# Kernel optimization log

Hardware: AMD Instinct MI355X
Metric: run time of the kernel (lower is better)

The kernel has to match this reference:

```python
import jax, jax.numpy as jnp
import numpy as np

U, B, S, R = 64, 256, 256, 512
N = 4096
EMA_DECAY = 0.99


def setup_inputs() -> dict:
    key = jax.random.key(0)
    ks = jax.random.split(key, 9)
    q_u = jax.random.uniform(ks[0], (N, U), dtype=jnp.float32)
    q_b = jax.random.uniform(ks[1], (N, B), dtype=jnp.float32)
    q_sigma = jax.random.normal(ks[2], (N, S), dtype=jnp.float32)
    delta_rule_target = jax.random.normal(ks[3], (N, R), dtype=jnp.float32)
    write_mask = jax.random.randint(ks[4], (N,), 0, 2).astype(bool)
    delta_rule_proto = 0.02 * jax.random.normal(ks[5], (U, B, R), dtype=jnp.float32)
    signature_proto = 0.02 * jax.random.normal(ks[6], (U, B, S), dtype=jnp.float32)
    ema_conf = jax.random.uniform(ks[7], (U, B), dtype=jnp.float32)
    usage_count = jnp.maximum(jax.random.uniform(ks[8], (U, B)) - 0.5, 0.0) * 100.0
    return {"q_u": q_u, "q_b": q_b, "q_sigma": q_sigma,
            "delta_rule_target": delta_rule_target, "write_mask": write_mask,
            "delta_rule_proto": delta_rule_proto, "signature_proto": signature_proto,
            "ema_conf": ema_conf, "usage_count": usage_count}


def _l2norm(x):
    return x / jnp.maximum(jnp.linalg.norm(x, axis=-1, keepdims=True), 1e-12)


def reference(q_u, q_b, q_sigma, delta_rule_target, write_mask,
              delta_rule_proto, signature_proto, ema_conf, usage_count):
    # ---------------- retrieve ----------------
    # joint attention over (operator, binding) cells; temperature == 1.0 branch
    joint = q_u[:, :, None] * q_b[:, None, :]                  # [N, U, B]
    valid = (usage_count > 0).astype(joint.dtype)              # [U, B]
    w = joint * valid
    denom = w.sum(axis=(-2, -1), keepdims=True)
    w = jnp.where(denom > 0, w / jnp.maximum(denom, 1e-6), jnp.zeros_like(w))
    memory_delta_rule = jnp.einsum('nub,ubr->nr', w, delta_rule_proto)
    memory_signature = jnp.einsum('nub,ubs->ns', w, signature_proto)
    base_conf = jnp.einsum('nub,ub->n', w, ema_conf)[:, None]  # [N, 1]
    cos = jnp.sum(_l2norm(q_sigma) * _l2norm(memory_signature + 1e-6),
                  axis=-1, keepdims=True)
    signature_agreement = 0.5 * (1.0 + cos)
    memory_conf = jnp.clip(base_conf * signature_agreement, 0.0, 1.0)

    # ---------------- update (vectorized scatter EMA) ----------------
    m = write_mask.astype(q_u.dtype)                           # [N]
    op_conf = q_u.max(axis=-1)
    op_id = jnp.argmax(q_u, axis=-1)
    bind_conf = q_b.max(axis=-1)
    bind_id = jnp.argmax(q_b, axis=-1)
    write_conf = op_conf * bind_conf                           # [N]
    cell = op_id * B + bind_id                                 # [N]
    num_cells = U * B
    wgt = write_conf * m
    sum_w = jax.ops.segment_sum(wgt, cell, num_segments=num_cells)          # [UB]
    sum_d = jax.ops.segment_sum(delta_rule_target * wgt[:, None], cell,
                                num_segments=num_cells)                     # [UB, R]
    sum_s = jax.ops.segment_sum(q_sigma * wgt[:, None], cell,
                                num_segments=num_cells)                     # [UB, S]
    cnt = jax.ops.segment_sum(m, cell, num_segments=num_cells)              # [UB]
    conf_sum = jnp.maximum(sum_w, 1e-6)
    delta_mean = (sum_d / conf_sum[:, None]).reshape(U, B, R)
    sigma_mean = (sum_s / conf_sum[:, None]).reshape(U, B, S)
    conf_mean = (sum_w / jnp.maximum(cnt, 1.0)).reshape(U, B)
    upd = (cnt > 0).reshape(U, B)
    new_delta_proto = jnp.where(upd[:, :, None],
                                EMA_DECAY * delta_rule_proto + (1.0 - EMA_DECAY) * delta_mean,
                                delta_rule_proto)
    new_signature_proto = jnp.where(upd[:, :, None],
                                    EMA_DECAY * signature_proto + (1.0 - EMA_DECAY) * sigma_mean,
                                    signature_proto)
    new_ema_conf = jnp.where(upd,
                             EMA_DECAY * ema_conf + (1.0 - EMA_DECAY) * conf_mean,
                             ema_conf)
    new_usage = usage_count + cnt.reshape(U, B)

    # ---------------- usage stats ----------------
    write_rate = m.mean()
    usage_fraction = (new_usage > 0).astype(jnp.float32).mean()
    dist = new_usage.reshape(-1)
    dist = dist / jnp.maximum(dist.sum(), 1e-6)
    usage_entropy = -(dist * jnp.log(dist + 1e-6)).sum() / np.log(max(2, num_cells))

    return (memory_delta_rule, memory_signature, memory_conf,
            new_delta_proto, new_signature_proto, new_ema_conf, new_usage,
            write_rate, usage_fraction, usage_entropy)
```

## Files before the change

### kernel.cpp

```cpp
#include <hip/hip_runtime.h>
#include <hip/hip_fp8.h>
#include <math.h>

#define NR 4096
#define UD 64
#define BD 256
#define SD 256
#define RD 512
#define UBD 16384
#define DECAY 0.99f

typedef unsigned char u8;
typedef __attribute__((ext_vector_type(4))) float f32x4;
typedef __attribute__((ext_vector_type(2))) long longx2;

#define OFF_MDR   0ull
#define OFF_MSIG  2097152ull
#define OFF_MCONF 3145728ull
#define OFF_NDP   3149824ull
#define OFF_NSP   11538432ull
#define OFF_NEC   15732736ull
#define OFF_NUS   15749120ull
#define OFF_SCAL  15765504ull

static __device__ __forceinline__ u8 f2e4m3(float x) {
  __hip_fp8_e4m3 h(x);
  return (u8)h.__x;
}

static __device__ __forceinline__ void gll16(const void* g, void* l) {
  __builtin_amdgcn_global_load_lds(
      (const __attribute__((address_space(1))) unsigned int*)g,
      (__attribute__((address_space(3))) unsigned int*)l, 16, 0, 0);
}

static __device__ __forceinline__ int perm64(int x) {
  return (((x >> 3) & 3) << 4) | (((x >> 5) & 1) << 3) | (x & 7);
}

__global__ __launch_bounds__(256) void row_prep_kernel(
    const float* __restrict__ q_u, const float* __restrict__ q_b,
    const float* __restrict__ usage, const float* __restrict__ ema,
    const unsigned char* __restrict__ wm,
    float* __restrict__ denom, float* __restrict__ base_raw,
    float* __restrict__ wgt, int* __restrict__ cellid, float* __restrict__ mrow)
{
  const int r0 = blockIdx.x * 4;
  const int t = threadIdx.x;
  __shared__ float s_qu[4][64];
  __shared__ float s_qbv[4][256];
  __shared__ float s_pd[4][256];
  __shared__ float s_pc[4][256];
  __shared__ int s_flag;
  {
    const int r = t >> 6, u = t & 63;
    s_qu[r][u] = q_u[(size_t)(r0 + r) * UD + u];
  }
  if (t == 0) {
    const int*   wi = (const int*)wm;
    const float* wf = (const float*)wm;
    bool is_i32 = true, is_f32 = true;
    #pragma unroll
    for (int i = 0; i < 16; ++i) {
      int v = wi[i];
      if (v != 0 && v != 1) is_i32 = false;
      float f = wf[i];
      if (f != 0.f && f != 1.f) is_f32 = false;
    }
    s_flag = is_i32 ? 2 : (is_f32 ? 1 : 0);
  }
  #pragma unroll
  for (int r = 0; r < 4; ++r)
    s_qbv[r][t] = q_b[(size_t)(r0 + r) * BD + t];
  __syncthreads();
  float accd[4] = {0.f, 0.f, 0.f, 0.f};
  float accc[4] = {0.f, 0.f, 0.f, 0.f};
  #pragma unroll 4
  for (int u = 0; u < UD; ++u) {
    const float us = usage[u * BD + t];
    const float em = ema[u * BD + t];
    const float vm = (us > 0.f) ? 1.f : 0.f;
    const float ev = em * vm;
    #pragma unroll
    for (int r = 0; r < 4; ++r) {
      accd[r] += s_qu[r][u] * vm;
      accc[r] += s_qu[r][u] * ev;
    }
  }
  #pragma unroll
  for (int r = 0; r < 4; ++r) {
    s_pd[r][t] = accd[r] * s_qbv[r][t];
    s_pc[r][t] = accc[r] * s_qbv[r][t];
  }
  __syncthreads();
  const int w = t >> 6, l = t & 63;
  float dsum = s_pd[w][l] + s_pd[w][l + 64] + s_pd[w][l + 128] + s_pd[w][l + 192];
  float csum = s_pc[w][l] + s_pc[w][l + 64] + s_pc[w][l + 128] + s_pc[w][l + 192];
  #pragma unroll
  for (int m = 1; m < 64; m <<= 1) {
    dsum += __shfl_xor(dsum, m);
    csum += __shfl_xor(csum, m);
  }
  float bv_ = s_qbv[w][l]; int bi_ = l;
  #pragma unroll
  for (int k = 1; k < 4; ++k) {
    const float v2 = s_qbv[w][l + k * 64];
    if (v2 > bv_) { bv_ = v2; bi_ = l + k * 64; }
  }
  #pragma unroll
  for (int m = 1; m < 64; m <<= 1) {
    const float ov = __shfl_xor(bv_, m);
    const int   oi = __shfl_xor(bi_, m);
    if (ov > bv_ || (ov == bv_ && oi < bi_)) { bv_ = ov; bi_ = oi; }
  }
  float uv_ = s_qu[w][l & 63]; int ui_ = l;
  #pragma unroll
  for (int m = 1; m < 64; m <<= 1) {
    const float ov = __shfl_xor(uv_, m);
    const int   oi = __shfl_xor(ui_, m);
    if (ov > uv_ || (ov == uv_ && oi < ui_)) { uv_ = ov; ui_ = oi; }
  }
  if (l == 0) {
    const int n = r0 + w;
    const int fm = s_flag;
    float m;
    if (fm == 2)      m = (((const int*)wm)[n]   != 0)   ? 1.f : 0.f;
    else if (fm == 1) m = (((const float*)wm)[n] != 0.f) ? 1.f : 0.f;
    else              m = (wm[n] != 0)   ? 1.f : 0.f;
    denom[n]    = dsum;
    base_raw[n] = csum;
    wgt[n]      = uv_ * bv_ * m;
    cellid[n]   = ui_ * BD + bi_;
    mrow[n]     = m;
  }
}

__global__ __launch_bounds__(256) void prep_kernel(
    const float* __restrict__ qb, const float* __restrict__ qu,
    u8* __restrict__ qb8, float* __restrict__ quT)
{
  if (blockIdx.x < 1024) {
    const int i = blockIdx.x * 256 + threadIdx.x;
    const int idx = i * 4;
    const int row = idx >> 8;
    const int b   = idx & 255;
    const float4 v = *(const float4*)(qb + (size_t)idx);
    u8 tmp[4] = { f2e4m3(v.x), f2e4m3(v.y), f2e4m3(v.z), f2e4m3(v.w) };
    unsigned int wv; __builtin_memcpy(&wv, tmp, 4);
    const int nb = (b & ~63) | perm64(b & 63);
    *(unsigned int*)(qb8 + (size_t)row * BD + nb) = wv;
  } else {
    __shared__ float s[64][65];
    const int n0 = (blockIdx.x - 1024) * 64;
    const int tid = threadIdx.x;
    #pragma unroll
    for (int i = 0; i < 16; ++i) {
      const int idx = tid + i * 256;
      const int r = idx >> 6, u = idx & 63;
      s[r][u] = qu[(size_t)(n0 + r) * UD + u];
    }
    __syncthreads();
    #pragma unroll
    for (int i = 0; i < 16; ++i) {
      const int idx = tid + i * 256;
      const int u = idx >> 6, r = idx & 63;
      quT[(size_t)u * NR + n0 + r] = s[r][u];
    }
  }
}

__global__ __launch_bounds__(256) void transpose_mask_kernel(
    const float* __restrict__ dproto, const float* __restrict__ sproto,
    const float* __restrict__ usage, u8* __restrict__ PT8)
{
  __shared__ u8 s[64][68];
  const int k0 = blockIdx.x * 64;
  const int rblk = blockIdx.y;
  const float* src; int ld; int c0s;
  if (rblk < 8) { src = dproto; ld = RD; c0s = rblk * 64; }
  else          { src = sproto; ld = SD; c0s = (rblk - 8) * 64; }
  const int tid = threadIdx.x;
  const int kl = tid >> 4;
  const int rl = (tid & 15) * 4;
  #pragma unroll
  for (int i = 0; i < 4; ++i) {
    const int k = kl + i * 16;
    const bool valid = usage[k0 + k] > 0.f;
    const float4 v = *(const float4*)(src + (size_t)(k0 + k) * ld + c0s + rl);
    s[k][rl + 0] = valid ? f2e4m3(v.x) : (u8)0;
    s[k][rl + 1] = valid ? f2e4m3(v.y) : (u8)0;
    s[k][rl + 2] = valid ? f2e4m3(v.z) : (u8)0;
    s[k][rl + 3] = valid ? f2e4m3(v.w) : (u8)0;
  }
  __syncthreads();
  const int rl2 = tid >> 4;
  const int kl2 = (tid & 15) * 4;
  #pragma unroll
  for (int i = 0; i < 4; ++i) {
    const int r = rl2 + i * 16;
    u8 tmp[4] = { s[kl2 + 0][r], s[kl2 + 1][r], s[kl2 + 2][r], s[kl2 + 3][r] };
    unsigned int wv; __builtin_memcpy(&wv, tmp, 4);
    *(unsigned int*)(PT8 + (size_t)(rblk * 64 + r) * UBD + k0 + perm64(kl2)) = wv;
  }
}

__global__ __launch_bounds__(256, 3) void mfma_gemm_kernel(
    const float* __restrict__ quT, const u8* __restrict__ qb8,
    const u8* __restrict__ PT8, float* __restrict__ out,
    int* __restrict__ tk, int* __restrict__ gf, int* __restrict__ claimed)
{
  __shared__ u8 sA[2][128 * 128];
  __shared__ u8 sB[2][128 * 64];
  __shared__ int s_work;
  const int tid = threadIdx.x;

  if (tid == 0) {
    unsigned int xcc;
    asm volatile("s_getreg_b32 %0, hwreg(HW_REG_XCC_ID)" : "=s"(xcc));
    const int x = (int)(xcc & 7u);
    const int t = atomicAdd(&tk[x], 1);
    int w = -1;
    if (t < 96) {
      const int cand = x * 96 + t;
      if (atomicCAS(&claimed[cand], 0, 1) == 0) w = cand;
    }
    while (w < 0) {
      const int g = atomicAdd(gf, 1);
      if (g >= 768) { w = -2; break; }
      if (atomicCAS(&claimed[g], 0, 1) == 0) w = g;
    }
    s_work = w;
  }
  __syncthreads();
  const int w = s_work;
  if (w < 0) return;

  const int bx = w & 31;
  const int combo = w >> 5;
  const int by = combo >> 2;
  const int bz = combo & 3;

  const int wid = tid >> 6, lane = tid & 63;
  const int n0 = bx * 128;
  const int kbeg = bz * (UBD / 4);

  float* obase; int ldO; int cc0;
  if (by < 4) { obase = out + OFF_MDR;  ldO = RD; cc0 = by * 128; }
  else        { obase = out + OFF_MSIG; ldO = SD; cc0 = (by - 4) * 128; }
  const int c0 = by * 128;

  const int lrowA = lane >> 3;
  const int csrcA = ((lane & 7) ^ lrowA) * 16;
  const u8* gA = qb8 + (size_t)(n0 + lrowA) * BD + csrcA;
  const int lrowB = lane >> 2;
  const int srcslotB = (lane & 3) ^ ((lrowB >> 1) & 3);
  const u8* gB = PT8 + (size_t)(c0 + wid * 16 + lrowB) * UBD + kbeg + srcslotB * 16;

  const int wr = (wid >> 1) * 64, wc = (wid & 1) * 64;
  const int fr = lane & 15;
  const int kg = lane >> 4;
  int aoff[4], boff[4];
  #pragma unroll
  for (int m = 0; m < 4; ++m) aoff[m] = (wr + m * 16 + fr) * 128;
  #pragma unroll
  for (int nn = 0; nn < 4; ++nn) boff[nn] = (wc + nn * 16 + fr) * 64;
  int slothA[2];
  #pragma unroll
  for (int bq = 0; bq < 2; ++bq) slothA[bq] = ((bq * 4 + kg) ^ (fr & 7)) * 16;
  const int slotB16 = (kg ^ ((fr >> 1) & 3)) * 16;

  f32x4 accm[4][4];
  #pragma unroll
  for (int m = 0; m < 4; ++m)
    #pragma unroll
    for (int nn = 0; nn < 4; ++nn)
      accm[m][nn] = (f32x4){0.f, 0.f, 0.f, 0.f};

  #pragma unroll
  for (int i = 0; i < 4; ++i) {
    const int ro = wid * 32 + i * 8;
    gll16(gA + (size_t)ro * BD,       &sA[0][ro * 128]);
    gll16(gA + (size_t)ro * BD + 128, &sA[1][ro * 128]);
  }
  #pragma unroll
  for (int i = 0; i < 2; ++i)
    gll16(gB + (size_t)(i * 64) * UBD, &sB[0][(i * 64 + wid * 16) * 64]);
  __syncthreads();

  const float* quTb = quT + n0 + wr + kg * 4;
  const int ubase = kbeg >> 8;
  f32x4 accu[4][4];

  for (int ph = 0; ph < 64; ++ph) {
    const int buf  = ph & 1;
    const int half = (ph >> 1) & 1;
    const int bq   = ph & 1;
    if (ph < 63) {
      const u8* gs = gB + (size_t)(ph + 1) * 64;
      #pragma unroll
      for (int i = 0; i < 2; ++i)
        gll16(gs + (size_t)(i * 64) * UBD, &sB[buf ^ 1][(i * 64 + wid * 16) * 64]);
    }
    const u8* sa = sA[half];
    const u8* sb = sB[buf];
    longx2 av[4], bv[4];
    #pragma unroll
    for (int m = 0; m < 4; ++m)
      av[m] = *(const longx2*)(sa + aoff[m] + slothA[bq]);
    #pragma unroll
    for (int nn = 0; nn < 4; ++nn)
      bv[nn] = *(const longx2*)(sb + boff[nn] + slotB16);
    const bool first = (ph & 3) == 0;
    #pragma unroll
    for (int m = 0; m < 4; ++m)
      #pragma unroll
      for (int nn = 0; nn < 4; ++nn) {
        if (first)
          accu[m][nn] = __builtin_amdgcn_mfma_f32_16x16x32_fp8_fp8(
              av[m].x, bv[nn].x, (f32x4){0.f, 0.f, 0.f, 0.f}, 0, 0, 0);
        else
          accu[m][nn] = __builtin_amdgcn_mfma_f32_16x16x32_fp8_fp8(
              av[m].x, bv[nn].x, accu[m][nn], 0, 0, 0);
        accu[m][nn] = __builtin_amdgcn_mfma_f32_16x16x32_fp8_fp8(
            av[m].y, bv[nn].y, accu[m][nn], 0, 0, 0);
      }
    __syncthreads();
    if ((ph & 3) == 3) {
      const float* qp = quTb + (size_t)(ubase + (ph >> 2)) * NR;
      #pragma unroll
      for (int m = 0; m < 4; ++m) {
        const f32x4 qv = *(const f32x4*)(qp + m * 16);
        #pragma unroll
        for (int nn = 0; nn < 4; ++nn)
          accm[m][nn] += qv * accu[m][nn];
      }
    }
  }

  #pragma unroll
  for (int m = 0; m < 4; ++m) {
    #pragma unroll
    for (int nn = 0; nn < 4; ++nn) {
      const int c = cc0 + wc + nn * 16 + fr;
      #pragma unroll
      for (int j = 0; j < 4; ++j) {
        const int r = n0 + wr + m * 16 + kg * 4 + j;
        atomicAdd(obase + (size_t)r * ldO + c, accm[m][nn][j]);
      }
    }
  }
}

__global__ __launch_bounds__(256) void epilogue_kernel(
    const float* __restrict__ q_sigma, const float* __restrict__ denom,
    const float* __restrict__ base_raw, float* __restrict__ out)
{
  const int n = blockIdx.x;
  const int t = threadIdx.x;
  __shared__ float r1[256], r2[256], r3[256];
  const float d = denom[n];
  const float scale = (d > 0.f) ? (1.f / fmaxf(d, 1e-6f)) : 0.f;
  float* mdr = out + OFF_MDR + (size_t)n * RD;
  mdr[t]       *= scale;
  mdr[t + 256] *= scale;
  float* msig = out + OFF_MSIG + (size_t)n * SD;
  const float s = msig[t] * scale;
  msig[t] = s;
  const float a = q_sigma[(size_t)n * SD + t];
  const float b = s + 1e-6f;
  r1[t] = a * a; r2[t] = b * b; r3[t] = a * b;
  __syncthreads();
  for (int st = 128; st > 0; st >>= 1) {
    if (t < st) { r1[t] += r1[t + st]; r2[t] += r2[t + st]; r3[t] += r3[t + st]; }
    __syncthreads();
  }
  if (t == 0) {
    const float na = fmaxf(sqrtf(r1[0]), 1e-12f);
    const float nb = fmaxf(sqrtf(r2[0]), 1e-12f);
    const float cosv = r3[0] / (na * nb);
    const float agree = 0.5f * (1.f + cosv);
    const float base = (d > 0.f) ? base_raw[n] / fmaxf(d, 1e-6f) : 0.f;
    out[OFF_MCONF + n] = fminf(fmaxf(base * agree, 0.f), 1.f);
  }
}

__global__ __launch_bounds__(256) void small_sums_kernel(
    const float* __restrict__ wgt, const int* __restrict__ cellid,
    const float* __restrict__ mrow,
    float* __restrict__ sum_w, float* __restrict__ cnt)
{
  const int n = blockIdx.x * 256 + threadIdx.x;
  if (n < NR && mrow[n] != 0.f) {
    atomicAdd(&sum_w[cellid[n]], wgt[n]);
    atomicAdd(&cnt[cellid[n]], 1.f);
  }
}

__global__ __launch_bounds__(256) void ema_copy_kernel(
    const float* __restrict__ dproto, const float* __restrict__ sproto,
    const float* __restrict__ cnt,
    float* __restrict__ outd, float* __restrict__ outs)
{
  const size_t nd = (size_t)UBD * RD;
  const size_t total = nd + (size_t)UBD * SD;
  for (size_t i = (size_t)blockIdx.x * 256 + threadIdx.x; i < total;
       i += (size_t)gridDim.x * 256) {
    if (i < nd) {
      const float p = dproto[i];
      outd[i] = (cnt[(int)(i >> 9)] > 0.f) ? DECAY * p : p;
    } else {
      const size_t j = i - nd;
      const float p = sproto[j];
      outs[j] = (cnt[(int)(j >> 8)] > 0.f) ? DECAY * p : p;
    }
  }
}

__global__ __launch_bounds__(256) void scatter2_kernel(
    const float* __restrict__ dtarget, const float* __restrict__ q_sigma,
    const float* __restrict__ wgt, const int* __restrict__ cellid,
    const float* __restrict__ mrow, const float* __restrict__ sum_w,
    float* __restrict__ outd, float* __restrict__ outs)
{
  const int n = blockIdx.x;
  if (mrow[n] == 0.f) return;
  const int t = threadIdx.x;
  const int c = cellid[n];
  const float cs = fmaxf(sum_w[c], 1e-6f);
  const float coef = (1.0f - DECAY) * wgt[n] / cs;
  atomicAdd(&outd[(size_t)c * RD + t],       dtarget[(size_t)n * RD + t] * coef);
  atomicAdd(&outd[(size_t)c * RD + t + 256], dtarget[(size_t)n * RD + t + 256] * coef);
  atomicAdd(&outs[(size_t)c * SD + t],       q_sigma[(size_t)n * SD + t] * coef);
}

__global__ __launch_bounds__(256) void ema_small_kernel(
    const float* __restrict__ ema, const float* __restrict__ usage,
    const float* __restrict__ sum_w, const float* __restrict__ cnt,
    float* __restrict__ out_ec, float* __restrict__ out_us)
{
  const int i = blockIdx.x * 256 + threadIdx.x;
  if (i < UBD) {
    const float c = cnt[i];
    const float cm = sum_w[i] / fmaxf(c, 1.f);
    out_ec[i] = (c > 0.f) ? DECAY * ema[i] + (1.f - DECAY) * cm : ema[i];
    out_us[i] = usage[i] + c;
  }
}

__global__ __launch_bounds__(256) void stats_kernel(
    const float* __restrict__ cnt, const float* __restrict__ new_us,
    float* __restrict__ out_scalars)
{
  const int t = threadIdx.x;
  __shared__ float r1[256], r2[256], r3[256];
  float scnt = 0.f, snz = 0.f, sus = 0.f;
  for (int i = t; i < UBD; i += 256) {
    const float c = cnt[i]; scnt += c;
    const float u = new_us[i];
    if (u > 0.f) snz += 1.f;
    sus += u;
  }
  r1[t] = scnt; r2[t] = snz; r3[t] = sus;
  __syncthreads();
  for (int s = 128; s > 0; s >>= 1) {
    if (t < s) { r1[t] += r1[t + s]; r2[t] += r2[t + s]; r3[t] += r3[t + s]; }
    __syncthreads();
  }
  const float total_cnt = r1[0], total_nz = r2[0], total_us = r3[0];
  __syncthreads();
  const float S = fmaxf(total_us, 1e-6f);
  float ent = 0.f;
  for (int i = t; i < UBD; i += 256) {
    const float d = new_us[i] / S;
    ent += d * logf(d + 1e-6f);
  }
  r1[t] = ent;
  __syncthreads();
  for (int s = 128; s > 0; s >>= 1) {
    if (t < s) { r1[t] += r1[t + s]; }
    __syncthreads();
  }
  if (t == 0) {
    out_scalars[0] = total_cnt / (float)NR;
    out_scalars[1] = total_nz / (float)UBD;
    out_scalars[2] = -r1[0] / 9.70406053f;
  }
}

extern "C" void kernel_launch(void* const* d_in, const int* in_sizes, int n_in,
                              void* d_out, int out_size, void* d_ws, size_t ws_size,
                              hipStream_t stream)
{
  const float* q_u    = (const float*)d_in[0];
  const float* q_b    = (const float*)d_in[1];
  const float* q_sig  = (const float*)d_in[2];
  const float* dtg    = (const float*)d_in[3];
  const unsigned char* wm = (const unsigned char*)d_in[4];
  const float* dproto = (const float*)d_in[5];
  const float* sproto = (const float*)d_in[6];
  const float* ema    = (const float*)d_in[7];
  const float* usage  = (const float*)d_in[8];
  float* out = (float*)d_out;

  float* wsf = (float*)d_ws;
  int*   wsi = (int*)d_ws;
  float* denom    = wsf + 16;
  float* base_raw = wsf + 16 + 4096;
  float* wgtb     = wsf + 16 + 8192;
  int*   cellid   = wsi + 16 + 12288;
  float* mrow     = wsf + 16 + 16384;
  float* sum_w    = wsf + 20496;
  float* cnt      = wsf + 20496 + 16384;
  int*   tk       = wsi + 53264;
  int*   gf       = wsi + 53272;
  int*   claimed  = wsi + 53280;

  u8*    PT8 = (u8*)(out + OFF_NDP);
  u8*    qb8 = PT8 + (size_t)768 * UBD;
  float* quT = (float*)(qb8 + (size_t)NR * BD);

  prep_kernel<<<1024 + NR / 64, 256, 0, stream>>>(q_b, q_u, qb8, quT);
  transpose_mask_kernel<<<dim3(UBD / 64, 12), 256, 0, stream>>>(dproto, sproto,
                                                                usage, PT8);
  hipMemsetAsync(out, 0, (size_t)OFF_MCONF * sizeof(float), stream);
  hipMemsetAsync(sum_w, 0, (2u * UBD + 16 + 768) * sizeof(float), stream);

  row_prep_kernel<<<NR / 4, 256, 0, stream>>>(q_u, q_b, usage, ema, wm,
                                              denom, base_raw, wgtb, cellid, mrow);
  small_sums_kernel<<<NR / 256, 256, 0, stream>>>(wgtb, cellid, mrow, sum_w, cnt);
  mfma_gemm_kernel<<<768, 256, 0, stream>>>(quT, qb8, PT8, out, tk, gf, claimed);
  epilogue_kernel<<<NR, 256, 0, stream>>>(q_sig, denom, base_raw, out);

  ema_copy_kernel<<<4096, 256, 0, stream>>>(dproto, sproto, cnt,
                                            out + OFF_NDP, out + OFF_NSP);
  scatter2_kernel<<<NR, 256, 0, stream>>>(dtg, q_sig, wgtb, cellid, mrow, sum_w,
                                          out + OFF_NDP, out + OFF_NSP);
  ema_small_kernel<<<UBD / 256, 256, 0, stream>>>(ema, usage, sum_w, cnt,
                                                  out + OFF_NEC, out + OFF_NUS);
  stats_kernel<<<1, 256, 0, stream>>>(cnt, out + OFF_NUS, out + OFF_SCAL);
}
```

Measured before the change: 214.0 us.

## Make GEMM persistent with triple-buffered B loads and fold small sums into row prep

After: 253.7 us. 18.6% more time.

```diff
diff --git a/kernel.cpp b/kernel.cpp
--- a/kernel.cpp
+++ b/kernel.cpp
@@ -43,7 +43,8 @@
     const float* __restrict__ usage, const float* __restrict__ ema,
     const unsigned char* __restrict__ wm,
     float* __restrict__ denom, float* __restrict__ base_raw,
-    float* __restrict__ wgt, int* __restrict__ cellid, float* __restrict__ mrow)
+    float* __restrict__ wgt, int* __restrict__ cellid, float* __restrict__ mrow,
+    float* __restrict__ sum_w, float* __restrict__ cnt)
 {
   const int r0 = blockIdx.x * 4;
   const int t = threadIdx.x;
@@ -127,11 +128,17 @@
     if (fm == 2)      m = (((const int*)wm)[n]   != 0)   ? 1.f : 0.f;
     else if (fm == 1) m = (((const float*)wm)[n] != 0.f) ? 1.f : 0.f;
     else              m = (wm[n] != 0)   ? 1.f : 0.f;
+    const float wv = uv_ * bv_ * m;
+    const int cell = ui_ * BD + bi_;
     denom[n]    = dsum;
     base_raw[n] = csum;
-    wgt[n]      = uv_ * bv_ * m;
-    cellid[n]   = ui_ * BD + bi_;
+    wgt[n]      = wv;
+    cellid[n]   = cell;
     mrow[n]     = m;
+    if (m != 0.f) {
+      atomicAdd(&sum_w[cell], wv);
+      atomicAdd(&cnt[cell], 1.f);
+    }
   }
 }
 
@@ -204,58 +211,21 @@
   }
 }
 
-__global__ __launch_bounds__(256, 3) void mfma_gemm_kernel(
+__global__ __launch_bounds__(256, 2) void mfma_gemm_kernel(
     const float* __restrict__ quT, const u8* __restrict__ qb8,
     const u8* __restrict__ PT8, float* __restrict__ out,
     int* __restrict__ tk, int* __restrict__ gf, int* __restrict__ claimed)
 {
   __shared__ u8 sA[2][128 * 128];
-  __shared__ u8 sB[2][128 * 64];
+  __shared__ u8 sB[3][128 * 64];
   __shared__ int s_work;
   const int tid = threadIdx.x;
-
-  if (tid == 0) {
-    unsigned int xcc;
-    asm volatile("s_getreg_b32 %0, hwreg(HW_REG_XCC_ID)" : "=s"(xcc));
-    const int x = (int)(xcc & 7u);
-    const int t = atomicAdd(&tk[x], 1);
-    int w = -1;
-    if (t < 96) {
-      const int cand = x * 96 + t;
-      if (atomicCAS(&claimed[cand], 0, 1) == 0) w = cand;
-    }
-    while (w < 0) {
-      const int g = atomicAdd(gf, 1);
-      if (g >= 768) { w = -2; break; }
-      if (atomicCAS(&claimed[g], 0, 1) == 0) w = g;
-    }
-    s_work = w;
-  }
-  __syncthreads();
-  const int w = s_work;
-  if (w < 0) return;
-
-  const int bx = w & 31;
-  const int combo = w >> 5;
-  const int by = combo >> 2;
-  const int bz = combo & 3;
-
   const int wid = tid >> 6, lane = tid & 63;
-  const int n0 = bx * 128;
-  const int kbeg = bz * (UBD / 4);
-
-  float* obase; int ldO; int cc0;
-  if (by < 4) { obase = out + OFF_MDR;  ldO = RD; cc0 = by * 128; }
-  else        { obase = out + OFF_MSIG; ldO = SD; cc0 = (by - 4) * 128; }
-  const int c0 = by * 128;
 
   const int lrowA = lane >> 3;
   const int csrcA = ((lane & 7) ^ lrowA) * 16;
-  const u8* gA = qb8 + (size_t)(n0 + lrowA) * BD + csrcA;
   const int lrowB = lane >> 2;
   const int srcslotB = (lane & 3) ^ ((lrowB >> 1) & 3);
-  const u8* gB = PT8 + (size_t)(c0 + wid * 16 + lrowB) * UBD + kbeg + srcslotB * 16;
-
   const int wr = (wid >> 1) * 64, wc = (wid & 1) * 64;
   const int fr = lane & 15;
   const int kg = lane >> 4;
@@ -269,83 +239,124 @@
   for (int bq = 0; bq < 2; ++bq) slothA[bq] = ((bq * 4 + kg) ^ (fr & 7)) * 16;
   const int slotB16 = (kg ^ ((fr >> 1) & 3)) * 16;
 
-  f32x4 accm[4][4];
-  #pragma unroll
-  for (int m = 0; m < 4; ++m)
-    #pragma unroll
-    for (int nn = 0; nn < 4; ++nn)
-      accm[m][nn] = (f32x4){0.f, 0.f, 0.f, 0.f};
-
-  #pragma unroll
-  for (int i = 0; i < 4; ++i) {
-    const int ro = wid * 32 + i * 8;
-    gll16(gA + (size_t)ro * BD,       &sA[0][ro * 128]);
-    gll16(gA + (size_t)ro * BD + 128, &sA[1][ro * 128]);
-  }
-  #pragma unroll
-  for (int i = 0; i < 2; ++i)
-    gll16(gB + (size_t)(i * 64) * UBD, &sB[0][(i * 64 + wid * 16) * 64]);
-  __syncthreads();
-
-  const float* quTb = quT + n0 + wr + kg * 4;
-  const int ubase = kbeg >> 8;
-  f32x4 accu[4][4];
-
-  for (int ph = 0; ph < 64; ++ph) {
-    const int buf  = ph & 1;
-    const int half = (ph >> 1) & 1;
-    const int bq   = ph & 1;
-    if (ph < 63) {
-      const u8* gs = gB + (size_t)(ph + 1) * 64;
-      #pragma unroll
-      for (int i = 0; i < 2; ++i)
-        gll16(gs + (size_t)(i * 64) * UBD, &sB[buf ^ 1][(i * 64 + wid * 16) * 64]);
-    }
-    const u8* sa = sA[half];
-    const u8* sb = sB[buf];
-    longx2 av[4], bv[4];
-    #pragma unroll
-    for (int m = 0; m < 4; ++m)
-      av[m] = *(const longx2*)(sa + aoff[m] + slothA[bq]);
-    #pragma unroll
-    for (int nn = 0; nn < 4; ++nn)
-      bv[nn] = *(const longx2*)(sb + boff[nn] + slotB16);
-    const bool first = (ph & 3) == 0;
+  for (;;) {
+    if (tid == 0) {
+      unsigned int xcc;
+      asm volatile("s_getreg_b32 %0, hwreg(HW_REG_XCC_ID)" : "=s"(xcc));
+      const int x = (int)(xcc & 7u);
+      const int t = atomicAdd(&tk[x], 1);
+      int w = -1;
+      if (t < 96) {
+        const int cand = x * 96 + t;
+        if (atomicCAS(&claimed[cand], 0, 1) == 0) w = cand;
+      }
+      while (w < 0) {
+        const int g = atomicAdd(gf, 1);
+        if (g >= 768) { w = -2; break; }
+        if (atomicCAS(&claimed[g], 0, 1) == 0) w = g;
+      }
+      s_work = w;
+    }
+    __syncthreads();
+    const int w = s_work;
+    if (w < 0) return;
+
+    const int bx = w & 31;
+    const int combo = w >> 5;
+    const int by = combo >> 2;
+    const int bz = combo & 3;
+
+    const int n0 = bx * 128;
+    const int kbeg = bz * (UBD / 4);
+
+    float* obase; int ldO; int cc0;
+    if (by < 4) { obase = out + OFF_MDR;  ldO = RD; cc0 = by * 128; }
+    else        { obase = out + OFF_MSIG; ldO = SD; cc0 = (by - 4) * 128; }
+    const int c0 = by * 128;
+
+    const u8* gA = qb8 + (size_t)(n0 + lrowA) * BD + csrcA;
+    const u8* gB = PT8 + (size_t)(c0 + wid * 16 + lrowB) * UBD + kbeg + srcslotB * 16;
+
+    f32x4 accm[4][4];
     #pragma unroll
     for (int m = 0; m < 4; ++m)
       #pragma unroll
+      for (int nn = 0; nn < 4; ++nn)
+        accm[m][nn] = (f32x4){0.f, 0.f, 0.f, 0.f};
+
+    #pragma unroll
+    for (int i = 0; i < 4; ++i) {
+      const int ro = wid * 32 + i * 8;
+      gll16(gA + (size_t)ro * BD,       &sA[0][ro * 128]);
+      gll16(gA + (size_t)ro * BD + 128, &sA[1][ro * 128]);
+    }
+    #pragma unroll
+    for (int i = 0; i < 2; ++i) {
+      gll16(gB + (size_t)(i * 64) * UBD,       &sB[0][(i * 64 + wid * 16) * 64]);
+      gll16(gB + (size_t)(i * 64) * UBD + 64,  &sB[1][(i * 64 + wid * 16) * 64]);
+    }
+
+    const float* quTb = quT + n0 + wr + kg * 4;
+    const int ubase = kbeg >> 8;
+    f32x4 accu[4][4];
+
+    for (int ph = 0; ph < 64; ++ph) {
+      if (ph == 63) asm volatile("s_waitcnt vmcnt(0)" ::: "memory");
+      else          asm volatile("s_waitcnt vmcnt(2)" ::: "memory");
+      __builtin_amdgcn_s_barrier();
+      if (ph < 62) {
+        const u8* gs = gB + (size_t)(ph + 2) * 64;
+        u8* ld = &sB[(ph + 2) % 3][wid * 16 * 64];
+        #pragma unroll
+        for (int i = 0; i < 2; ++i)
+          gll16(gs + (size_t)(i * 64) * UBD, ld + i * 64 * 64);
+      }
+      const u8* sa = sA[(ph >> 1) & 1];
+      const u8* sb = sB[ph % 3];
+      const int bq = ph & 1;
+      longx2 av[4], bv[4];
+      #pragma unroll
+      for (int m = 0; m < 4; ++m)
+        av[m] = *(const longx2*)(sa + aoff[m] + slothA[bq]);
+      #pragma unroll
+      for (int nn = 0; nn < 4; ++nn)
+        bv[nn] = *(const longx2*)(sb + boff[nn] + slotB16);
+      const bool first = (ph & 3) == 0;
+      #pragma unroll
+      for (int m = 0; m < 4; ++m)
+        #pragma unroll
+        for (int nn = 0; nn < 4; ++nn) {
+          if (first)
+            accu[m][nn] = __builtin_amdgcn_mfma_f32_16x16x32_fp8_fp8(
+                av[m].x, bv[nn].x, (f32x4){0.f, 0.f, 0.f, 0.f}, 0, 0, 0);
+          else
+            accu[m][nn] = __builtin_amdgcn_mfma_f32_16x16x32_fp8_fp8(
+                av[m].x, bv[nn].x, accu[m][nn], 0, 0, 0);
+          accu[m][nn] = __builtin_amdgcn_mfma_f32_16x16x32_fp8_fp8(
+              av[m].y, bv[nn].y, accu[m][nn], 0, 0, 0);
+        }
+      if ((ph & 3) == 3) {
+        const float* qp = quTb + (size_t)(ubase + (ph >> 2)) * NR;
+        #pragma unroll
+        for (int m = 0; m < 4; ++m) {
+          const f32x4 qv = *(const f32x4*)(qp + m * 16);
+          #pragma unroll
+          for (int nn = 0; nn < 4; ++nn)
+            accm[m][nn] += qv * accu[m][nn];
+        }
+      }
+    }
+
+    #pragma unroll
+    for (int m = 0; m < 4; ++m) {
+      #pragma unroll
       for (int nn = 0; nn < 4; ++nn) {
-        if (first)
-          accu[m][nn] = __builtin_amdgcn_mfma_f32_16x16x32_fp8_fp8(
-              av[m].x, bv[nn].x, (f32x4){0.f, 0.f, 0.f, 0.f}, 0, 0, 0);
-        else
-          accu[m][nn] = __builtin_amdgcn_mfma_f32_16x16x32_fp8_fp8(
-              av[m].x, bv[nn].x, accu[m][nn], 0, 0, 0);
-        accu[m][nn] = __builtin_amdgcn_mfma_f32_16x16x32_fp8_fp8(
-            av[m].y, bv[nn].y, accu[m][nn], 0, 0, 0);
-      }
-    __syncthreads();
-    if ((ph & 3) == 3) {
-      const float* qp = quTb + (size_t)(ubase + (ph >> 2)) * NR;
-      #pragma unroll
-      for (int m = 0; m < 4; ++m) {
-        const f32x4 qv = *(const f32x4*)(qp + m * 16);
+        const int c = cc0 + wc + nn * 16 + fr;
         #pragma unroll
-        for (int nn = 0; nn < 4; ++nn)
-          accm[m][nn] += qv * accu[m][nn];
-      }
-    }
-  }
-
-  #pragma unroll
-  for (int m = 0; m < 4; ++m) {
-    #pragma unroll
-    for (int nn = 0; nn < 4; ++nn) {
-      const int c = cc0 + wc + nn * 16 + fr;
-      #pragma unroll
-      for (int j = 0; j < 4; ++j) {
-        const int r = n0 + wr + m * 16 + kg * 4 + j;
-        atomicAdd(obase + (size_t)r * ldO + c, accm[m][nn][j]);
+        for (int j = 0; j < 4; ++j) {
+          const int r = n0 + wr + m * 16 + kg * 4 + j;
+          atomicAdd(obase + (size_t)r * ldO + c, accm[m][nn][j]);
+        }
       }
     }
   }
@@ -384,18 +395,6 @@
   }
 }
 
-__global__ __launch_bounds__(256) void small_sums_kernel(
-    const float* __restrict__ wgt, const int* __restrict__ cellid,
-    const float* __restrict__ mrow,
-    float* __restrict__ sum_w, float* __restrict__ cnt)
-{
-  const int n = blockIdx.x * 256 + threadIdx.x;
-  if (n < NR && mrow[n] != 0.f) {
-    atomicAdd(&sum_w[cellid[n]], wgt[n]);
-    atomicAdd(&cnt[cellid[n]], 1.f);
-  }
-}
-
 __global__ __launch_bounds__(256) void ema_copy_kernel(
     const float* __restrict__ dproto, const float* __restrict__ sproto,
     const float* __restrict__ cnt,
@@ -526,9 +525,9 @@
   hipMemsetAsync(sum_w, 0, (2u * UBD + 16 + 768) * sizeof(float), stream);
 
   row_prep_kernel<<<NR / 4, 256, 0, stream>>>(q_u, q_b, usage, ema, wm,
-                                              denom, base_raw, wgtb, cellid, mrow);
-  small_sums_kernel<<<NR / 256, 256, 0, stream>>>(wgtb, cellid, mrow, sum_w, cnt);
-  mfma_gemm_kernel<<<768, 256, 0, stream>>>(quT, qb8, PT8, out, tk, gf, claimed);
+                                              denom, base_raw, wgtb, cellid, mrow,
+                                              sum_w, cnt);
+  mfma_gemm_kernel<<<512, 256, 0, stream>>>(quT, qb8, PT8, out, tk, gf, claimed);
   epilogue_kernel<<<NR, 256, 0, stream>>>(q_sig, denom, base_raw, out);
 
   ema_copy_kernel<<<4096, 256, 0, stream>>>(dproto, sproto, cnt,
```
